# Optimization experiments

Hardware: AMD Instinct MI355X
Metric: run time of the kernel (lower is better)

Reference implementation:

```python
import jax, jax.numpy as jnp
import numpy as np

N, F_IN, F_OUT = 8192, 512, 256


def setup_inputs() -> dict:
    key = jax.random.key(0)
    k1, k2, k3, k4 = jax.random.split(key, 4)
    x = jax.random.normal(k1, (N, F_IN), dtype=jnp.float32)
    adj = jax.random.randint(k2, (N, N), 0, 2, dtype=jnp.int32)
    # xavier-uniform-like init scale for W and a
    wb = 1.414 * np.sqrt(6.0 / (F_IN + F_OUT))
    ab = 1.414 * np.sqrt(6.0 / (2 * F_OUT + 1))
    W = jax.random.uniform(k3, (F_IN, F_OUT), minval=-wb, maxval=wb, dtype=jnp.float32)
    a = jax.random.uniform(k4, (2 * F_OUT, 1), minval=-ab, maxval=ab, dtype=jnp.float32)
    return {"x": x, "adj": adj, "W": W, "a": a, "heads": 4}


def reference(x, adj, W, a, heads):
    # Wh = x @ W : [N, F_OUT]
    Wh = x @ W
    f_out = W.shape[1]
    # a = [a_src; a_dst], so e_ij = leakyrelu(Wh_i . a_src + Wh_j . a_dst)
    s_src = Wh @ a[:f_out, 0]   # [N]
    s_dst = Wh @ a[f_out:, 0]   # [N]
    e = jax.nn.leaky_relu(s_src[:, None] + s_dst[None, :], negative_slope=0.2)  # [N, N]
    # scatter into dense matrix: non-edges hold 0 and DO participate in softmax
    att = jnp.where(adj != 0, e, jnp.zeros((), dtype=e.dtype))
    att = jax.nn.softmax(att, axis=1)
    # dropout is identity in eval mode (self.training=False)
    h = att @ Wh                                  # [N, F_OUT]
    n = x.shape[0]
    h = h.reshape(n, heads, f_out // heads).mean(axis=1)  # multi-head mean
    return h
```

## Files before the change

kernel.cpp:

```cpp
#include <hip/hip_runtime.h>
#include <hip/hip_bf16.h>

#define NN 8192
#define FIN 512
#define FOUT 256
#define FH 64
#define JSPLIT 16
#define JCHUNK 512
#define STEPS 8

typedef float f32x16 __attribute__((ext_vector_type(16)));
typedef short bf16x8 __attribute__((ext_vector_type(8)));
typedef unsigned short us8 __attribute__((ext_vector_type(8)));
typedef unsigned int uint32x4 __attribute__((ext_vector_type(4)));

static __device__ __forceinline__ unsigned short f2bf(float x) {
  unsigned int u = __builtin_bit_cast(unsigned int, x);
  unsigned int r = (u + 0x7fffu + ((u >> 16) & 1u)) >> 16;
  return (unsigned short)r;
}
static __device__ __forceinline__ float bf2f(unsigned short u) {
  unsigned int v = ((unsigned int)u) << 16;
  return __builtin_bit_cast(float, v);
}
static __device__ __forceinline__ float fastexp2(float x) {
  float r;
  asm("v_exp_f32 %0, %1" : "=v"(r) : "v"(x));
  return r;
}
static __device__ __forceinline__ unsigned int pkbf(float a, float b) {
  unsigned int w;
  asm("v_cvt_pk_bf16_f32 %0, %1, %2" : "=v"(w) : "v"(a), "v"(b));
  return w;
}
static __device__ __forceinline__ float lo16f(unsigned int w) {
  return __builtin_bit_cast(float, w << 16);
}
static __device__ __forceinline__ float hi16f(unsigned int w) {
  return __builtin_bit_cast(float, w & 0xffff0000u);
}
static __device__ __forceinline__ unsigned int ext4(int l31,
    unsigned long long c0, unsigned long long c1,
    unsigned long long c2, unsigned long long c3) {
  unsigned long long s01 = (l31 & 8) ? c1 : c0;
  unsigned long long s23 = (l31 & 8) ? c3 : c2;
  unsigned long long s = (l31 & 16) ? s23 : s01;
  return (unsigned int)(s >> ((l31 & 7) * 8)) & 0xffu;
}

__global__ __launch_bounds__(256) void prep_small(const float* __restrict__ W,
                                                  const float* __restrict__ a,
                                                  unsigned short* __restrict__ Bw) {
  const int kt = blockIdx.x;
  __shared__ float wm[16][64];
  __shared__ float wt[16][2];
  const int t = threadIdx.x;
#pragma unroll
  for (int i = 0; i < 4; ++i) {
    const int idx = t + i * 256;
    const int kr = idx >> 6, c = idx & 63;
    const float* wr = W + (size_t)(kt * 16 + kr) * FOUT + c;
    wm[kr][c] = 0.25f * (wr[0] + wr[64] + wr[128] + wr[192]);
  }
  if (t < 32) {
    const int kr = t & 15, sel = t >> 4;
    const float* wr = W + (size_t)(kt * 16 + kr) * FOUT;
    const float* av = a + sel * FOUT;
    float s = 0.f;
    for (int n = 0; n < FOUT; ++n) s += wr[n] * av[n];
    wt[kr][sel] = s * 1.44269504f;
  }
  __syncthreads();
#pragma unroll
  for (int i = 0; i < 12; ++i) {
    const int idx = t + i * 256;
    const int e = idx & 7, n = (idx >> 3) & 31, r2 = idx >> 8;
    const int khb = r2 & 1, q = r2 >> 1;
    const int nf = q % 3, h = q / 3;
    const int k = khb * 8 + e;
    float v = nf < 2 ? wm[k][nf * 32 + n]
                     : (n == 0 ? wt[k][0] : (n == 1 ? wt[k][1] : 0.f));
    const unsigned short hi = f2bf(v);
    Bw[(size_t)kt * 3072 + idx] = (h == 0) ? hi : f2bf(v - bf2f(hi));
  }
}

__global__ __launch_bounds__(192) void gemm_whm(const float* __restrict__ X,
                                                const unsigned short* __restrict__ Bw,
                                                unsigned short* __restrict__ Bg,
                                                float* __restrict__ ssrc,
                                                float* __restrict__ sdst) {
  __shared__ float xs[32][516];
  __shared__ float sred[32][2];
  const int mw = blockIdx.x;
  const int tid = threadIdx.x;
  const float* xb = X + (size_t)(mw * 32) * FIN;
  for (int i = tid; i < 4096; i += 192) {
    const int row = i >> 7, c4 = (i & 127) << 2;
    *(float4*)&xs[row][c4] = *(const float4*)(xb + (size_t)row * FIN + c4);
  }
  __syncthreads();

  const int nf = tid >> 6, lane = tid & 63;
  const int l31 = lane & 31, kh = lane >> 5;
  f32x16 acc = (f32x16)(0.f);
  const unsigned short* bp = Bw + ((size_t)nf * 2 + kh) * 256 + l31 * 8;
#pragma unroll 4
  for (int kt = 0; kt < 32; ++kt) {
    const float* xr = &xs[l31][kt * 16 + kh * 8];
    const float4 va = *(const float4*)xr;
    const float4 vb = *(const float4*)(xr + 4);
    const unsigned int h0 = pkbf(va.x, va.y), h1 = pkbf(va.z, va.w);
    const unsigned int h2 = pkbf(vb.x, vb.y), h3 = pkbf(vb.z, vb.w);
    const unsigned int l0 = pkbf(va.x - lo16f(h0), va.y - hi16f(h0));
    const unsigned int l1 = pkbf(va.z - lo16f(h1), va.w - hi16f(h1));
    const unsigned int l2 = pkbf(vb.x - lo16f(h2), vb.y - hi16f(h2));
    const unsigned int l3 = pkbf(vb.z - lo16f(h3), vb.w - hi16f(h3));
    const uint32x4 uh = {h0, h1, h2, h3}, ul = {l0, l1, l2, l3};
    const bf16x8 a_h = __builtin_bit_cast(bf16x8, uh);
    const bf16x8 a_l = __builtin_bit_cast(bf16x8, ul);
    const bf16x8 b_h = *(const bf16x8*)(bp + kt * 3072);
    const bf16x8 b_l = *(const bf16x8*)(bp + kt * 3072 + 1536);
    acc = __builtin_amdgcn_mfma_f32_32x32x16_bf16(a_h, b_h, acc, 0, 0, 0);
    acc = __builtin_amdgcn_mfma_f32_32x32x16_bf16(a_h, b_l, acc, 0, 0, 0);
    acc = __builtin_amdgcn_mfma_f32_32x32x16_bf16(a_l, b_h, acc, 0, 0, 0);
  }
  if (nf < 2) {
    unsigned short* bgw = Bg + (size_t)mw * 2048;
#pragma unroll
    for (int reg = 0; reg < 16; reg += 2) {
      const unsigned int wh = pkbf(acc[reg], acc[reg + 1]);
      const int e = (reg & 3) | (kh << 2);
      const int khb = (reg >> 2) & 1;
      const int kc = reg >> 3;
      *(unsigned int*)(bgw + (size_t)(((kc * 2 + khb) * 2 + nf) * 256) +
                       l31 * 8 + e) = wh;
    }
  } else if (l31 < 2) {
#pragma unroll
    for (int reg = 0; reg < 16; ++reg) {
      const int row = (reg & 3) + ((reg >> 2) << 3) + (kh << 2);
      sred[row][l31] = acc[reg];
    }
  }
  __syncthreads();
  if (threadIdx.x < 32) {
    ssrc[mw * 32 + threadIdx.x] = sred[threadIdx.x][0];
    sdst[mw * 32 + threadIdx.x] = sred[threadIdx.x][1];
  }
}

#define GLL(G, L)                                                           \
  __builtin_amdgcn_global_load_lds(                                         \
      (const __attribute__((address_space(1))) unsigned int*)(G),           \
      (__attribute__((address_space(3))) unsigned int*)(L), 16, 0, 0)

#define PEL(P, MM, B, SD)                    \
  float P;                                   \
  {                                          \
    float tt = ss + (SD);                    \
    float lr = fmaxf(tt, 0.2f * tt);         \
    lr = (((MM) >> (B)) & 1u) ? lr : 0.0f;   \
    P = fastexp2(lr);                        \
    dacc += P;                               \
  }

#define GENAF(AF, M0, M1, M2, M3, KC4, SA, SB)                            \
  {                                                                       \
    PEL(p0, M0, (KC4) + 0, (SA).x) PEL(p1, M1, (KC4) + 0, (SA).y)         \
    PEL(p2, M2, (KC4) + 0, (SA).z) PEL(p3, M3, (KC4) + 0, (SA).w)         \
    PEL(p4, M0, (KC4) + 1, (SB).x) PEL(p5, M1, (KC4) + 1, (SB).y)         \
    PEL(p6, M2, (KC4) + 1, (SB).z) PEL(p7, M3, (KC4) + 1, (SB).w)         \
    const uint32x4 uv = {pkbf(p0, p1), pkbf(p2, p3), pkbf(p4, p5),        \
                         pkbf(p6, p7)};                                   \
    AF = __builtin_bit_cast(bf16x8, uv);                                  \
  }

__global__ __launch_bounds__(1024, 4) void gat_aggr(
    const int* __restrict__ adj, const float* __restrict__ ssrc_g,
    const float* __restrict__ sdst_g, const unsigned short* __restrict__ Bg,
    unsigned short* __restrict__ Upb, float* __restrict__ Dp) {
  __shared__ unsigned short lbuf[16 * 2048];
  __shared__ float sds[768];
  const int bid = blockIdx.x;
  const int bj = bid & 15, bm = bid >> 4;
  const int wv = threadIdx.x >> 6, lane = threadIdx.x & 63;
  const int wvr = wv & 7, jhalf = wv >> 3;
  const int l31 = lane & 31, kh = lane >> 5;
  const int rbase = bm * 256;
  const int myrow = rbase + wvr * 32 + l31;
  const int jb = bj * JCHUNK + jhalf * 256;
  const float ss = ssrc_g[myrow];

  {
    const unsigned short* gs =
        Bg + (size_t)(bj * 16 + wv) * 2048 + lane * 8;
#pragma unroll
    for (int c = 0; c < 4; ++c) GLL(gs + c * 512, &lbuf[wv * 2048 + c * 512]);
    if (wv == 0) {
      GLL(sdst_g + bj * JCHUNK + lane * 4, &sds[0]);
      GLL(sdst_g + bj * JCHUNK + 256 + lane * 4, &sds[256]);
    }
  }

  const int* astep = adj + (size_t)(rbase + wvr * 32 + (lane >> 3)) * NN + jb +
                     (lane & 7) * 4;
  int4 qa0 = *(const int4*)(astep + (size_t)0 * 8 * NN);
  int4 qa1 = *(const int4*)(astep + (size_t)1 * 8 * NN);
  int4 qa2 = *(const int4*)(astep + (size_t)2 * 8 * NN);
  int4 qa3 = *(const int4*)(astep + (size_t)3 * 8 * NN);
  int4 qb0 = *(const int4*)(astep + (size_t)0 * 8 * NN + 32);
  int4 qb1 = *(const int4*)(astep + (size_t)1 * 8 * NN + 32);
  int4 qb2 = *(const int4*)(astep + (size_t)2 * 8 * NN + 32);
  int4 qb3 = *(const int4*)(astep + (size_t)3 * 8 * NN + 32);

  f32x16 acc0 = (f32x16)(0.f), acc1 = (f32x16)(0.f);
  float dacc = 0.f;
  __syncthreads();

  const unsigned short* lb0 = &lbuf[(jhalf * 8) * 2048 + kh * 512 + l31 * 8];
  const float* sdl = &sds[jhalf * 256 + kh * 8];
  const int kh2 = kh * 2;

#define PSTEP(T, QS0, QS1, QS2, QS3, RELOAD)                                  \
  {                                                                          \
    const unsigned int mk0 = ext4(l31, __ballot((QS0).x != 0),               \
        __ballot((QS1).x != 0), __ballot((QS2).x != 0), __ballot((QS3).x != 0)); \
    const unsigned int mk1 = ext4(l31, __ballot((QS0).y != 0),               \
        __ballot((QS1).y != 0), __ballot((QS2).y != 0), __ballot((QS3).y != 0)); \
    const unsigned int mk2 = ext4(l31, __ballot((QS0).z != 0),               \
        __ballot((QS1).z != 0), __ballot((QS2).z != 0), __ballot((QS3).z != 0)); \
    const unsigned int mk3 = ext4(l31, __ballot((QS0).w != 0),               \
        __ballot((QS1).w != 0), __ballot((QS2).w != 0), __ballot((QS3).w != 0)); \
    if (RELOAD) {                                                            \
      const int* an = astep + ((T) + 2) * 32;                                \
      QS0 = *(const int4*)(an + (size_t)0 * 8 * NN);                         \
      QS1 = *(const int4*)(an + (size_t)1 * 8 * NN);                         \
      QS2 = *(const int4*)(an + (size_t)2 * 8 * NN);                         \
      QS3 = *(const int4*)(an + (size_t)3 * 8 * NN);                         \
    }                                                                        \
    const unsigned int m0 = mk0 >> kh2, m1 = mk1 >> kh2;                     \
    const unsigned int m2 = mk2 >> kh2, m3 = mk3 >> kh2;                     \
    const unsigned short* tb = lb0 + (size_t)(T) * 2048;                     \
    const bf16x8 b00 = *(const bf16x8*)(tb);                    \
    const bf16x8 b01 = *(const bf16x8*)(tb + 256);              \
    const bf16x8 b10 = *(const bf16x8*)(tb + 1024);             \
    const bf16x8 b11 = *(const bf16x8*)(tb + 1280);             \
    const float4 sA0 = *(const float4*)(sdl + (T) * 32);                     \
    const float4 sB0 = *(const float4*)(sdl + (T) * 32 + 4);                 \
    const float4 sA1 = *(const float4*)(sdl + (T) * 32 + 16);                \
    const float4 sB1 = *(const float4*)(sdl + (T) * 32 + 20);                \
    bf16x8 af0, af1;                                                         \
    GENAF(af0, m0, m1, m2, m3, 0, sA0, sB0)                                  \
    GENAF(af1, m0, m1, m2, m3, 4, sA1, sB1)                                  \
    acc0 = __builtin_amdgcn_mfma_f32_32x32x16_bf16(af0, b00, acc0, 0, 0, 0); \
    acc1 = __builtin_amdgcn_mfma_f32_32x32x16_bf16(af0, b01, acc1, 0, 0, 0); \
    acc0 = __builtin_amdgcn_mfma_f32_32x32x16_bf16(af1, b10, acc0, 0, 0, 0); \
    acc1 = __builtin_amdgcn_mfma_f32_32x32x16_bf16(af1, b11, acc1, 0, 0, 0); \
  }

#pragma unroll 1
  for (int it = 0; it < 3; ++it) {
    const int t0 = 2 * it;
    PSTEP(t0, qa0, qa1, qa2, qa3, 1)
    PSTEP(t0 + 1, qb0, qb1, qb2, qb3, 1)
  }
  PSTEP(6, qa0, qa1, qa2, qa3, 0)
  PSTEP(7, qb0, qb1, qb2, qb3, 0)
#undef PSTEP

  dacc += __shfl_xor(dacc, 32);
  __syncthreads();
  float* lf = (float*)lbuf;
  const int slot = wvr * 2048;
  if (jhalf) {
#pragma unroll
    for (int r = 0; r < 16; ++r) lf[slot + r * 64 + lane] = acc0[r];
#pragma unroll
    for (int r = 0; r < 16; ++r) lf[slot + (16 + r) * 64 + lane] = acc1[r];
    if (lane < 32) sds[512 + wvr * 32 + l31] = dacc;
  }
  __syncthreads();
  if (jhalf) return;
#pragma unroll
  for (int r = 0; r < 16; ++r) acc0[r] += lf[slot + r * 64 + lane];
#pragma unroll
  for (int r = 0; r < 16; ++r) acc1[r] += lf[slot + (16 + r) * 64 + lane];
  dacc += sds[512 + wvr * 32 + l31];

  if (lane < 32) Dp[(size_t)bj * NN + myrow] = dacc;

  unsigned short* ub = Upb + ((size_t)bj * NN + rbase + wvr * 32) * FH;
#pragma unroll
  for (int reg = 0; reg < 16; ++reg) {
    const int rr = (reg & 3) + ((reg >> 2) << 3) + (kh << 2);
    ub[(size_t)rr * FH + l31] = f2bf(acc0[reg]);
    ub[(size_t)rr * FH + 32 + l31] = f2bf(acc1[reg]);
  }
}

__global__ __launch_bounds__(256) void finalize(const unsigned short* __restrict__ Upb,
                                                const float* __restrict__ Dp,
                                                float* __restrict__ out) {
  const int idx2 = blockIdx.x * 256 + threadIdx.x;
  const int i = idx2 >> 5;
  const int c2 = (idx2 & 31) * 2;
  const size_t base = (size_t)i * FH + c2;
  float u0 = 0.f, u1 = 0.f, d = 0.f;
#pragma unroll
  for (int s = 0; s < JSPLIT; ++s) {
    d += Dp[(size_t)s * NN + i];
    const unsigned int w =
        *(const unsigned int*)(Upb + (size_t)s * NN * FH + base);
    u0 += bf2f((unsigned short)(w & 0xffffu));
    u1 += bf2f((unsigned short)(w >> 16));
  }
  const float inv = 1.0f / d;
  *(float2*)(out + base) = make_float2(u0 * inv, u1 * inv);
}

extern "C" void kernel_launch(void* const* d_in, const int* in_sizes, int n_in,
                              void* d_out, int out_size, void* d_ws, size_t ws_size,
                              hipStream_t stream) {
  const float* x = (const float*)d_in[0];
  const int* adj = (const int*)d_in[1];
  const float* W = (const float*)d_in[2];
  const float* a = (const float*)d_in[3];
  char* ws = (char*)d_ws;

  unsigned short* Upb = (unsigned short*)ws;
  unsigned short* Bg = (unsigned short*)(ws + ((size_t)32 << 20));
  unsigned short* Bw = (unsigned short*)(ws + ((size_t)36 << 20));
  float* ssrc = (float*)(ws + ((size_t)36 << 20) + (256u << 10));
  float* sdst = (float*)(ws + ((size_t)36 << 20) + (288u << 10));
  float* Dp = (float*)(ws + ((size_t)36 << 20) + (320u << 10));
  float* out = (float*)d_out;

  prep_small<<<32, 256, 0, stream>>>(W, a, Bw);
  gemm_whm<<<256, 192, 0, stream>>>(x, Bw, Bg, ssrc, sdst);
  gat_aggr<<<32 * JSPLIT, 1024, 0, stream>>>(adj, ssrc, sdst, Bg, Upb, Dp);
  finalize<<<NN * FH / 512, 256, 0, stream>>>(Upb, Dp, out);
}
```

Measured before the change: 82.76 us.

## Load adjacency in 64-column row slabs to halve reload rounds and ballot extraction

Each wave now reads the adjacency tile with 16 lanes per row, so every int4 load covers 64 columns of 4 rows instead of 32 columns of 8 rows. Each ballot group of eight loads yields masks for two MFMA steps, selected with a three-level mux. This halves the number of reload rounds and mask-extraction passes, and the loop is now fully unrolled. The cost is twice as many live int4 registers for the adjacency prefetch, which could raise register pressure or lower occupancy.

```diff
diff --git a/kernel.cpp b/kernel.cpp
--- a/kernel.cpp
+++ b/kernel.cpp
@@ -7,7 +7,6 @@
 #define FH 64
 #define JSPLIT 16
 #define JCHUNK 512
-#define STEPS 8
 
 typedef float f32x16 __attribute__((ext_vector_type(16)));
 typedef short bf16x8 __attribute__((ext_vector_type(8)));
@@ -39,13 +38,17 @@
 static __device__ __forceinline__ float hi16f(unsigned int w) {
   return __builtin_bit_cast(float, w & 0xffff0000u);
 }
-static __device__ __forceinline__ unsigned int ext4(int l31,
-    unsigned long long c0, unsigned long long c1,
-    unsigned long long c2, unsigned long long c3) {
-  unsigned long long s01 = (l31 & 8) ? c1 : c0;
-  unsigned long long s23 = (l31 & 8) ? c3 : c2;
-  unsigned long long s = (l31 & 16) ? s23 : s01;
-  return (unsigned int)(s >> ((l31 & 7) * 8)) & 0xffu;
+static __device__ __forceinline__ unsigned long long sel8(int i,
+    unsigned long long a0, unsigned long long a1, unsigned long long a2,
+    unsigned long long a3, unsigned long long a4, unsigned long long a5,
+    unsigned long long a6, unsigned long long a7) {
+  unsigned long long s0 = (i & 1) ? a1 : a0;
+  unsigned long long s1 = (i & 1) ? a3 : a2;
+  unsigned long long s2 = (i & 1) ? a5 : a4;
+  unsigned long long s3 = (i & 1) ? a7 : a6;
+  unsigned long long t0 = (i & 2) ? s1 : s0;
+  unsigned long long t1 = (i & 2) ? s3 : s2;
+  return (i & 4) ? t1 : t0;
 }
 
 __global__ __launch_bounds__(256) void prep_small(const float* __restrict__ W,
@@ -203,16 +206,24 @@
     }
   }
 
-  const int* astep = adj + (size_t)(rbase + wvr * 32 + (lane >> 3)) * NN + jb +
-                     (lane & 7) * 4;
-  int4 qa0 = *(const int4*)(astep + (size_t)0 * 8 * NN);
-  int4 qa1 = *(const int4*)(astep + (size_t)1 * 8 * NN);
-  int4 qa2 = *(const int4*)(astep + (size_t)2 * 8 * NN);
-  int4 qa3 = *(const int4*)(astep + (size_t)3 * 8 * NN);
-  int4 qb0 = *(const int4*)(astep + (size_t)0 * 8 * NN + 32);
-  int4 qb1 = *(const int4*)(astep + (size_t)1 * 8 * NN + 32);
-  int4 qb2 = *(const int4*)(astep + (size_t)2 * 8 * NN + 32);
-  int4 qb3 = *(const int4*)(astep + (size_t)3 * 8 * NN + 32);
+  const int* astep = adj + (size_t)(rbase + wvr * 32 + (lane >> 4)) * NN + jb +
+                     (lane & 15) * 4;
+  int4 qa0 = *(const int4*)(astep + (size_t)0 * 4 * NN);
+  int4 qa1 = *(const int4*)(astep + (size_t)1 * 4 * NN);
+  int4 qa2 = *(const int4*)(astep + (size_t)2 * 4 * NN);
+  int4 qa3 = *(const int4*)(astep + (size_t)3 * 4 * NN);
+  int4 qa4 = *(const int4*)(astep + (size_t)4 * 4 * NN);
+  int4 qa5 = *(const int4*)(astep + (size_t)5 * 4 * NN);
+  int4 qa6 = *(const int4*)(astep + (size_t)6 * 4 * NN);
+  int4 qa7 = *(const int4*)(astep + (size_t)7 * 4 * NN);
+  int4 qb0 = *(const int4*)(astep + (size_t)0 * 4 * NN + 64);
+  int4 qb1 = *(const int4*)(astep + (size_t)1 * 4 * NN + 64);
+  int4 qb2 = *(const int4*)(astep + (size_t)2 * 4 * NN + 64);
+  int4 qb3 = *(const int4*)(astep + (size_t)3 * 4 * NN + 64);
+  int4 qb4 = *(const int4*)(astep + (size_t)4 * 4 * NN + 64);
+  int4 qb5 = *(const int4*)(astep + (size_t)5 * 4 * NN + 64);
+  int4 qb6 = *(const int4*)(astep + (size_t)6 * 4 * NN + 64);
+  int4 qb7 = *(const int4*)(astep + (size_t)7 * 4 * NN + 64);
 
   f32x16 acc0 = (f32x16)(0.f), acc1 = (f32x16)(0.f);
   float dacc = 0.f;
@@ -221,26 +232,13 @@
   const unsigned short* lb0 = &lbuf[(jhalf * 8) * 2048 + kh * 512 + l31 * 8];
   const float* sdl = &sds[jhalf * 256 + kh * 8];
   const int kh2 = kh * 2;
-
-#define PSTEP(T, QS0, QS1, QS2, QS3, RELOAD)                                  \
+  const int g16 = (l31 & 3) * 16;
+  const int isel = l31 >> 2;
+
+#define CSTEP(T, MK0, MK1, MK2, MK3)                                          \
   {                                                                          \
-    const unsigned int mk0 = ext4(l31, __ballot((QS0).x != 0),               \
-        __ballot((QS1).x != 0), __ballot((QS2).x != 0), __ballot((QS3).x != 0)); \
-    const unsigned int mk1 = ext4(l31, __ballot((QS0).y != 0),               \
-        __ballot((QS1).y != 0), __ballot((QS2).y != 0), __ballot((QS3).y != 0)); \
-    const unsigned int mk2 = ext4(l31, __ballot((QS0).z != 0),               \
-        __ballot((QS1).z != 0), __ballot((QS2).z != 0), __ballot((QS3).z != 0)); \
-    const unsigned int mk3 = ext4(l31, __ballot((QS0).w != 0),               \
-        __ballot((QS1).w != 0), __ballot((QS2).w != 0), __ballot((QS3).w != 0)); \
-    if (RELOAD) {                                                            \
-      const int* an = astep + ((T) + 2) * 32;                                \
-      QS0 = *(const int4*)(an + (size_t)0 * 8 * NN);                         \
-      QS1 = *(const int4*)(an + (size_t)1 * 8 * NN);                         \
-      QS2 = *(const int4*)(an + (size_t)2 * 8 * NN);                         \
-      QS3 = *(const int4*)(an + (size_t)3 * 8 * NN);                         \
-    }                                                                        \
-    const unsigned int m0 = mk0 >> kh2, m1 = mk1 >> kh2;                     \
-    const unsigned int m2 = mk2 >> kh2, m3 = mk3 >> kh2;                     \
+    const unsigned int m0 = (MK0) >> kh2, m1 = (MK1) >> kh2;                 \
+    const unsigned int m2 = (MK2) >> kh2, m3 = (MK3) >> kh2;                 \
     const unsigned short* tb = lb0 + (size_t)(T) * 2048;                     \
     const bf16x8 b00 = *(const bf16x8*)(tb);                    \
     const bf16x8 b01 = *(const bf16x8*)(tb + 256);              \
@@ -259,15 +257,47 @@
     acc1 = __builtin_amdgcn_mfma_f32_32x32x16_bf16(af1, b11, acc1, 0, 0, 0); \
   }
 
-#pragma unroll 1
-  for (int it = 0; it < 3; ++it) {
-    const int t0 = 2 * it;
-    PSTEP(t0, qa0, qa1, qa2, qa3, 1)
-    PSTEP(t0 + 1, qb0, qb1, qb2, qb3, 1)
-  }
-  PSTEP(6, qa0, qa1, qa2, qa3, 0)
-  PSTEP(7, qb0, qb1, qb2, qb3, 0)
-#undef PSTEP
+#define SSTEP(S, Q0, Q1, Q2, Q3, Q4, Q5, Q6, Q7, RELOAD)                      \
+  {                                                                          \
+    const unsigned long long sx = sel8(isel,                                 \
+        __ballot((Q0).x != 0), __ballot((Q1).x != 0), __ballot((Q2).x != 0), \
+        __ballot((Q3).x != 0), __ballot((Q4).x != 0), __ballot((Q5).x != 0), \
+        __ballot((Q6).x != 0), __ballot((Q7).x != 0)) >> g16;                \
+    const unsigned long long sy = sel8(isel,                                 \
+        __ballot((Q0).y != 0), __ballot((Q1).y != 0), __ballot((Q2).y != 0), \
+        __ballot((Q3).y != 0), __ballot((Q4).y != 0), __ballot((Q5).y != 0), \
+        __ballot((Q6).y != 0), __ballot((Q7).y != 0)) >> g16;                \
+    const unsigned long long sz = sel8(isel,                                 \
+        __ballot((Q0).z != 0), __ballot((Q1).z != 0), __ballot((Q2).z != 0), \
+        __ballot((Q3).z != 0), __ballot((Q4).z != 0), __ballot((Q5).z != 0), \
+        __ballot((Q6).z != 0), __ballot((Q7).z != 0)) >> g16;                \
+    const unsigned long long sw = sel8(isel,                                 \
+        __ballot((Q0).w != 0), __ballot((Q1).w != 0), __ballot((Q2).w != 0), \
+        __ballot((Q3).w != 0), __ballot((Q4).w != 0), __ballot((Q5).w != 0), \
+        __ballot((Q6).w != 0), __ballot((Q7).w != 0)) >> g16;                \
+    if (RELOAD) {                                                            \
+      const int* an = astep + ((S) + 2) * 64;                                \
+      Q0 = *(const int4*)(an + (size_t)0 * 4 * NN);                          \
+      Q1 = *(const int4*)(an + (size_t)1 * 4 * NN);                          \
+      Q2 = *(const int4*)(an + (size_t)2 * 4 * NN);                          \
+      Q3 = *(const int4*)(an + (size_t)3 * 4 * NN);                          \
+      Q4 = *(const int4*)(an + (size_t)4 * 4 * NN);                          \
+      Q5 = *(const int4*)(an + (size_t)5 * 4 * NN);                          \
+      Q6 = *(const int4*)(an + (size_t)6 * 4 * NN);                          \
+      Q7 = *(const int4*)(an + (size_t)7 * 4 * NN);                          \
+    }                                                                        \
+    CSTEP(2 * (S), (unsigned int)sx, (unsigned int)sy, (unsigned int)sz,     \
+          (unsigned int)sw)                                                  \
+    CSTEP(2 * (S) + 1, (unsigned int)(sx >> 8), (unsigned int)(sy >> 8),     \
+          (unsigned int)(sz >> 8), (unsigned int)(sw >> 8))                  \
+  }
+
+  SSTEP(0, qa0, qa1, qa2, qa3, qa4, qa5, qa6, qa7, 1)
+  SSTEP(1, qb0, qb1, qb2, qb3, qb4, qb5, qb6, qb7, 1)
+  SSTEP(2, qa0, qa1, qa2, qa3, qa4, qa5, qa6, qa7, 0)
+  SSTEP(3, qb0, qb1, qb2, qb3, qb4, qb5, qb6, qb7, 0)
+#undef SSTEP
+#undef CSTEP
 
   dacc += __shfl_xor(dacc, 32);
   __syncthreads();
```

New measurement: 96.62 us. 16.7% more time.
